# Optimization experiments

Hardware: AMD Instinct MI355X
Metric: run time of the kernel (lower is better)

The kernel has to match this reference:

```python
import jax, jax.numpy as jnp
import numpy as np

GRID_DIMS = (64, 64, 64)
GRID_LOWER = np.array([0.0, 0.0, 0.0], np.float32)
GRID_STEPS = np.array([0.015625, 0.015625, 0.015625], np.float32)
RADIUS = 0.03125
STENCIL = 2  # ceil(radius / step)


def _poly6(d2, h):
    # standard SPH poly6 smoothing kernel: 315/(64 pi h^9) (h^2 - d^2)^3, d <= h
    c = np.float32(315.0 / (64.0 * np.pi * h ** 9))
    return jnp.where(d2 <= h * h, c * (h * h - d2) ** 3, 0.0)


def particles2grid(locs, data, density):
    # locs [B,N,3], data [B,N,C], density [B,N] -> grid [B,X,Y,Z,C]
    B, N, _ = locs.shape
    C = data.shape[-1]
    X, Y, Z = GRID_DIMS
    dims = jnp.array(GRID_DIMS, jnp.int32)
    r = jnp.arange(-STENCIL, STENCIL + 1)
    offs = jnp.stack(jnp.meshgrid(r, r, r, indexing='ij'), -1).reshape(-1, 3)  # [K,3]
    base = jnp.floor((locs - GRID_LOWER) / GRID_STEPS).astype(jnp.int32)        # [B,N,3]
    cells = base[:, :, None, :] + offs                                          # [B,N,K,3]
    centers = GRID_LOWER + (cells.astype(locs.dtype) + 0.5) * GRID_STEPS
    d2 = jnp.sum((centers - locs[:, :, None, :]) ** 2, -1)                      # [B,N,K]
    w = _poly6(d2, RADIUS)
    w = jnp.where(jnp.all((cells >= 0) & (cells < dims), -1), w, 0.0)
    contrib = w[..., None] * (data / density[..., None])[:, :, None, :]         # [B,N,K,C]
    cells = jnp.clip(cells, 0, dims - 1)
    flat = (cells[..., 0] * Y + cells[..., 1]) * Z + cells[..., 2]              # [B,N,K]

    def splat(f, c):
        return jnp.zeros((X * Y * Z, C), data.dtype).at[f.reshape(-1)].add(c.reshape(-1, C))

    return jax.vmap(splat)(flat, contrib).reshape(B, X, Y, Z, C)


def grid2particles(grid, locs):
    # trilinear interpolation of grid [B,X,Y,Z,C] at particle locations [B,N,3]
    B, X, Y, Z, C = grid.shape
    dims = jnp.array([X, Y, Z], jnp.int32)
    pos = (locs - GRID_LOWER) / GRID_STEPS - 0.5                                # cell-center coords
    i0 = jnp.floor(pos).astype(jnp.int32)
    frac = pos - i0.astype(locs.dtype)
    gflat = grid.reshape(B, X * Y * Z, C)
    gather = jax.vmap(lambda g, f: g[f])                                        # [B,N] -> [B,N,C]
    out = jnp.zeros((B, locs.shape[1], C), grid.dtype)
    for dx in (0, 1):
        for dy in (0, 1):
            for dz in (0, 1):
                off = jnp.array([dx, dy, dz], jnp.int32)
                idx = i0 + off
                wd = jnp.where(off == 1, frac, 1.0 - frac)                      # [B,N,3]
                w = wd[..., 0] * wd[..., 1] * wd[..., 2]
                w = jnp.where(jnp.all((idx >= 0) & (idx < dims), -1), w, 0.0)
                idx = jnp.clip(idx, 0, dims - 1)
                flat = (idx[..., 0] * Y + idx[..., 1]) * Z + idx[..., 2]
                out = out + w[..., None] * gather(gflat, flat)
    return out


def conv3d(x, w, b):
    y = jax.lax.conv_general_dilated(x, w, (1, 1, 1), 'SAME',
                                     dimension_numbers=('NCDHW', 'OIDHW', 'NCDHW'))
    return y + b[None, :, None, None, None]


def prelu(x, a):
    return jnp.where(x >= 0, x, a * x)


def setup_inputs() -> dict:
    key = jax.random.key(0)
    ks = jax.random.split(key, 8)
    B, N = 2, 32768
    Cin, K, Cout = 4, 32, 4
    s = lambda fan: np.float32(1.0 / np.sqrt(fan * 27))
    return {
        'locs': jax.random.uniform(ks[0], (B, N, 3), jnp.float32),
        'data': jax.random.normal(ks[1], (B, N, Cin), jnp.float32),
        'density': jax.random.uniform(ks[2], (B, N), jnp.float32, 0.5, 1.5),
        'W0': jax.random.normal(ks[3], (K, Cin, 3, 3, 3), jnp.float32) * s(Cin),
        'b0': jnp.zeros((K,), jnp.float32),
        'W1': jax.random.normal(ks[4], (K, K, 3, 3, 3), jnp.float32) * s(K),
        'b1': jnp.zeros((K,), jnp.float32),
        'W2': jax.random.normal(ks[5], (K, K, 3, 3, 3), jnp.float32) * s(K),
        'b2': jnp.zeros((K,), jnp.float32),
        'W3': jax.random.normal(ks[6], (Cout, K, 3, 3, 3), jnp.float32) * s(K),
        'b3': jnp.zeros((Cout,), jnp.float32),
        'a0': jnp.full((1,), 0.25, jnp.float32),
        'a1': jnp.full((1,), 0.25, jnp.float32),
        'a2': jnp.full((1,), 0.25, jnp.float32),
    }


def reference(locs, data, density, W0, b0, W1, b1, W2, b2, W3, b3, a0, a1, a2):
    grid = particles2grid(locs, data, density)            # [B,X,Y,Z,Cin]
    g = jnp.transpose(grid, (0, 4, 1, 2, 3))              # NCDHW
    g = prelu(conv3d(g, W0, b0), a0)
    g = prelu(conv3d(g, W1, b1), a1)
    g = prelu(conv3d(g, W2, b2), a2)
    g = conv3d(g, W3, b3)
    g = jnp.transpose(g, (0, 2, 3, 4, 1))                 # [B,X,Y,Z,Cout]
    return grid2particles(g, locs)                        # [B,N,Cout]
```

## Files before the change

kernel.cpp:

```cpp
#include <hip/hip_runtime.h>

#define BATCH 2
#define NPART 32768
#define GD 64
#define NVOX (BATCH * GD * GD * GD)

typedef unsigned short ushortT;
typedef __attribute__((ext_vector_type(8))) short short8;
typedef __attribute__((ext_vector_type(16))) float float16;

__device__ __forceinline__ float poly6_c() {
    const double H9 = 1.0 / 35184372088832.0;
    return (float)(315.0 / (64.0 * 3.14159265358979323846 * H9));
}

__device__ __forceinline__ ushortT bf16_rne(float f) {
    unsigned int u = __float_as_uint(f);
    u = (u + 0x7fffu + ((u >> 16) & 1u)) >> 16;
    return (ushortT)u;
}

__device__ __forceinline__ int imax(int a, int b) { return a > b ? a : b; }
__device__ __forceinline__ int imin(int a, int b) { return a < b ? a : b; }

__device__ __forceinline__ void load_lds16(const void* g, void* l) {
    __builtin_amdgcn_global_load_lds(
        (const __attribute__((address_space(1))) void*)g,
        (__attribute__((address_space(3))) void*)l, 16, 0, 0);
}

__device__ __forceinline__ int perm_ktL(int slot) {
    int g = slot / 6, r = slot - g * 6;
    int dy = r >> 1, p = r & 1;
    int dx = g / 3, dz = g - dx * 3;
    return (dx * 9 + dy * 3 + dz) * 2 + p;
}

__global__ __launch_bounds__(256) void prep_kernel(
    int* __restrict__ zp,
    const float* __restrict__ W0, const float* __restrict__ W1,
    const float* __restrict__ W2, const float* __restrict__ W3,
    short* __restrict__ Bp) {
    int bid = blockIdx.x, tid = threadIdx.x;
    if (bid < 513) {
        int t = bid * 256 + tid;
        if (t < 131088) zp[t] = 0;
        return;
    }
    int t = (bid - 513) * 256 + tid;
    if (t >= 176 * 512) return;
    int kt = t >> 9;
    const float* W; int O, I, CINP, ktL;
    if (kt < 14)       { W = W0; O = 32; I = 4;  CINP = 8;  ktL = kt; }
    else if (kt < 68)  { W = W1; O = 32; I = 32; CINP = 32; ktL = perm_ktL(kt - 14); }
    else if (kt < 122) { W = W2; O = 32; I = 32; CINP = 32; ktL = perm_ktL(kt - 68); }
    else               { W = W3; O = 4;  I = 32; CINP = 32; ktL = perm_ktL(kt - 122); }
    int l = (t >> 3) & 63, j = t & 7;
    int n = l & 31, q = l >> 5;
    int k = ktL * 16 + 8 * q + j;
    int tap = k / CINP;
    int ic  = k - tap * CINP;
    float v = 0.f;
    if (tap < 27 && ic < I && n < O) v = W[(n * I + ic) * 27 + tap];
    Bp[t] = (short)bf16_rne(v);
}

__global__ __launch_bounds__(256) void bin_count_kernel(
    const float* __restrict__ locs, int* __restrict__ counts) {
    int t = blockIdx.x * blockDim.x + threadIdx.x;
    if (t >= BATCH * NPART) return;
    int b = t >> 15;
    int bx = ((int)floorf(locs[t * 3 + 0] * 64.0f)) >> 1;
    int by = ((int)floorf(locs[t * 3 + 1] * 64.0f)) >> 1;
    int bz = ((int)floorf(locs[t * 3 + 2] * 64.0f)) >> 1;
    atomicAdd(&counts[b * 32768 + ((bx * 32) + by) * 32 + bz], 1);
}

__global__ __launch_bounds__(256) void scanA_kernel(
    const int* __restrict__ counts, int* __restrict__ offsets,
    int* __restrict__ blockSum) {
    __shared__ int sh[256];
    int tid = threadIdx.x, g = blockIdx.x;
    int v = counts[g * 256 + tid];
    sh[tid] = v;
    __syncthreads();
    for (int off = 1; off < 256; off <<= 1) {
        int u = (tid >= off) ? sh[tid - off] : 0;
        __syncthreads();
        sh[tid] += u;
        __syncthreads();
    }
    offsets[g * 256 + tid] = sh[tid] - v;
    if (tid == 255) blockSum[g] = sh[255];
}

__global__ __launch_bounds__(256) void scanB_kernel(
    int* __restrict__ offsets, const int* __restrict__ blockSum) {
    __shared__ int sh[256];
    int tid = threadIdx.x, g = blockIdx.x;
    sh[tid] = (tid < g) ? blockSum[tid] : 0;
    __syncthreads();
    for (int off = 128; off > 0; off >>= 1) {
        if (tid < off) sh[tid] += sh[tid + off];
        __syncthreads();
    }
    offsets[g * 256 + tid] += sh[0];
    if (g == 255 && tid == 255) offsets[65536] = BATCH * NPART;
}

__global__ __launch_bounds__(256) void bin_scatter_kernel(
    const float* __restrict__ locs, const float* __restrict__ data,
    const float* __restrict__ density, const int* __restrict__ offsets,
    int* __restrict__ cursor, float* __restrict__ payload) {
    int t = blockIdx.x * blockDim.x + threadIdx.x;
    if (t >= BATCH * NPART) return;
    int b = t >> 15;
    float px = locs[t * 3 + 0];
    float py = locs[t * 3 + 1];
    float pz = locs[t * 3 + 2];
    int bx = ((int)floorf(px * 64.0f)) >> 1;
    int by = ((int)floorf(py * 64.0f)) >> 1;
    int bz = ((int)floorf(pz * 64.0f)) >> 1;
    int bb = b * 32768 + ((bx * 32) + by) * 32 + bz;
    int slot = atomicAdd(&cursor[bb], 1);
    int idx = offsets[bb] + slot;
    float inv_d = 1.0f / density[t];
    float4 p0 = {px, py, pz, data[t * 4 + 0] * inv_d};
    float4 p1 = {data[t * 4 + 1] * inv_d, data[t * 4 + 2] * inv_d,
                 data[t * 4 + 3] * inv_d, 0.f};
    *(float4*)(payload + idx * 8)     = p0;
    *(float4*)(payload + idx * 8 + 4) = p1;
}

__global__ __launch_bounds__(256) void splat_gather_kernel(
    const float* __restrict__ payload, const int* __restrict__ offsets,
    ushortT* __restrict__ g8) {
    __shared__ float plist[256 * 8];
    __shared__ int segS[36];
    __shared__ int segP[37];
    __shared__ int shTot[1];

    int wg = blockIdx.x;
    int sb = wg & 511, b = wg >> 9;
    int X0 = (sb >> 6) * 8, Y0 = ((sb >> 3) & 7) * 8, Z0 = (sb & 7) * 8;
    int tid = threadIdx.x;

    int bxlo = imax(0, (X0 - 2) >> 1), bxhi = imin(31, (X0 + 9) >> 1);
    int bylo = imax(0, (Y0 - 2) >> 1), byhi = imin(31, (Y0 + 9) >> 1);
    int bzlo = imax(0, (Z0 - 2) >> 1), bzhi = imin(31, (Z0 + 9) >> 1);
    int ny = byhi - bylo + 1;
    int ns = (bxhi - bxlo + 1) * ny;
    if (tid < ns) {
        int bx = bxlo + tid / ny, by = bylo + tid % ny;
        int row = b * 32768 + (bx * 32 + by) * 32;
        int s = offsets[row + bzlo];
        int e = offsets[row + bzhi + 1];
        segS[tid] = s;
        segP[tid] = e - s;
    }
    __syncthreads();
    if (tid == 0) {
        int p = 0;
        for (int k = 0; k < ns; ++k) { int len = segP[k]; segP[k] = p; p += len; }
        segP[ns] = p;
        shTot[0] = p;
    }
    __syncthreads();

    const float step = 0.015625f;
    const float h2 = 0.03125f * 0.03125f;
    const float cc = poly6_c();
    int total = shTot[0];

    int l = tid & 63, w = tid >> 6;
    int cx = X0 + 4 * (w >> 1) + (l >> 4);
    int cy = Y0 + 4 * (w & 1) + ((l >> 2) & 3);
    int cz0 = Z0 + (l & 3);
    float xc  = ((float)cx  + 0.5f) * step;
    float yc  = ((float)cy  + 0.5f) * step;
    float zc0 = ((float)cz0 + 0.5f) * step;
    float zc1 = zc0 + 4.0f * step;

    float a00 = 0.f, a01 = 0.f, a02 = 0.f, a03 = 0.f;
    float a10 = 0.f, a11 = 0.f, a12 = 0.f, a13 = 0.f;

    int nchunks = (total + 255) >> 8;
    for (int ch = 0; ch < nchunks; ++ch) {
        __syncthreads();
        int jj = (ch << 8) + tid;
        if (jj < total) {
            int k = 0;
            while (jj >= segP[k + 1]) ++k;
            int idx = segS[k] + (jj - segP[k]);
            *(float4*)(plist + tid * 8)     = *(const float4*)(payload + idx * 8);
            *(float4*)(plist + tid * 8 + 4) = *(const float4*)(payload + idx * 8 + 4);
        }
        __syncthreads();
        int cnt = imin(256, total - (ch << 8));
        for (int p = 0; p < cnt; ++p) {
            float4 pa = *(const float4*)(plist + p * 8);
            float dx = pa.x - xc, dy = pa.y - yc;
            float dxy2 = fmaf(dy, dy, dx * dx);
            if (!__any(dxy2 <= h2)) continue;
            float4 pv = *(const float4*)(plist + p * 8 + 4);
            float dz0 = pa.z - zc0;
            float d20 = fmaf(dz0, dz0, dxy2);
            float u0 = fmaxf(h2 - d20, 0.f);
            float w0 = (cc * u0) * (u0 * u0);
            a00 = fmaf(w0, pa.w, a00);
            a01 = fmaf(w0, pv.x, a01);
            a02 = fmaf(w0, pv.y, a02);
            a03 = fmaf(w0, pv.z, a03);
            float dz1 = pa.z - zc1;
            float d21 = fmaf(dz1, dz1, dxy2);
            float u1 = fmaxf(h2 - d21, 0.f);
            float w1 = (cc * u1) * (u1 * u1);
            a10 = fmaf(w1, pa.w, a10);
            a11 = fmaf(w1, pv.x, a11);
            a12 = fmaf(w1, pv.y, a12);
            a13 = fmaf(w1, pv.z, a13);
        }
    }

    size_t cellBase = (size_t)(((b * 64 + cx) * 64 + cy) * 64);
    short8 o;
    o[0] = (short)bf16_rne(a00); o[1] = (short)bf16_rne(a01);
    o[2] = (short)bf16_rne(a02); o[3] = (short)bf16_rne(a03);
    o[4] = 0; o[5] = 0; o[6] = 0; o[7] = 0;
    *(short8*)(g8 + (cellBase + cz0) * 8) = o;
    o[0] = (short)bf16_rne(a10); o[1] = (short)bf16_rne(a11);
    o[2] = (short)bf16_rne(a12); o[3] = (short)bf16_rne(a13);
    *(short8*)(g8 + (cellBase + cz0 + 4) * 8) = o;
}

template <int ICG, int KT, bool FINAL>
__global__ __launch_bounds__(256, (ICG == 1) ? 3 : 2) void mfma_conv_kernel(
    const ushortT* __restrict__ in, const short* __restrict__ Bpack,
    const float* __restrict__ bias, const float* __restrict__ alpha,
    const float* __restrict__ zguard, void* __restrict__ outv) {
    constexpr int CIN = ICG * 8;
    constexpr int NCH = 36 * ICG * 34;
    __shared__ short lds[NCH * 8];
    int wg = ((blockIdx.x & 7) << 7) | (blockIdx.x >> 3);
    int zh = wg & 1, yq = (wg >> 1) & 15, xp = (wg >> 5) & 15, b = wg >> 9;
    int X0 = xp * 4, Y0 = yq * 4, Z0 = zh * 32;
    int tid = threadIdx.x;

    const ushortT* inb = in + (size_t)b * (64 * 64 * 64 * CIN);
#pragma unroll
    for (int it = 0; it < (NCH + 255) / 256; ++it) {
        int ccid = it * 256 + tid;
        if (ccid < NCH) {
            int col = ccid / (ICG * 34);
            int rem = ccid - col * (ICG * 34);
            int icg = rem / 34;
            int zi  = rem - icg * 34;
            int gx = X0 + col / 6 - 1;
            int gy = Y0 + col % 6 - 1;
            int gz = Z0 + zi - 1;
            const void* src = (const void*)zguard;
            if ((unsigned)gx < 64u && (unsigned)gy < 64u && (unsigned)gz < 64u)
                src = (const void*)(inb + ((size_t)(((gx * 64) + gy) * 64 + gz)) * CIN + icg * 8);
            load_lds16(src, (void*)(lds + ccid * 8));
        }
    }
    __syncthreads();

    int l = tid & 63, w = tid >> 6;
    int n = l & 31, q = l >> 5;

    float bval = FINAL ? (n < 4 ? bias[n] : 0.f) : bias[n];
    float16 acc0, acc1, acc2, acc3;
#pragma unroll
    for (int r = 0; r < 16; ++r) {
        acc0[r] = bval; acc1[r] = bval; acc2[r] = bval; acc3[r] = bval;
    }

    const short* bp = Bpack + (size_t)l * 8;
    int laneZ = (l & 31) * 8;

    short8 bf[4];
#pragma unroll
    for (int i = 0; i < 4; ++i) bf[i] = *(const short8*)(bp + i * 512);

    if constexpr (ICG == 1) {
#pragma unroll
        for (int kt = 0; kt < KT; ++kt) {
            short8 bcur = bf[kt & 3];
            if (kt + 4 < KT) bf[kt & 3] = *(const short8*)(bp + (kt + 4) * 512);
            int tap0 = kt * 2, tap1 = kt * 2 + 1;
            if (tap1 > 26) tap1 = 26;
            int dx0 = tap0 / 9, r0 = tap0 - dx0 * 9, dy0 = r0 / 3, dz0 = r0 - dy0 * 3;
            int dx1 = tap1 / 9, r1 = tap1 - dx1 * 9, dy1 = r1 / 3, dz1 = r1 - dy1 * 3;
#define AOFS1(c) (q ? ((((w + dx1) * 6 + ((c) + dy1)) * 34 + dz1) * 8) \
                    : ((((w + dx0) * 6 + ((c) + dy0)) * 34 + dz0) * 8))
            short8 a0 = *(const short8*)(lds + AOFS1(0) + laneZ);
            short8 a1 = *(const short8*)(lds + AOFS1(1) + laneZ);
            short8 a2 = *(const short8*)(lds + AOFS1(2) + laneZ);
            short8 a3 = *(const short8*)(lds + AOFS1(3) + laneZ);
#undef AOFS1
            __builtin_amdgcn_s_setprio(1);
            acc0 = __builtin_amdgcn_mfma_f32_32x32x16_bf16(a0, bcur, acc0, 0, 0, 0);
            acc1 = __builtin_amdgcn_mfma_f32_32x32x16_bf16(a1, bcur, acc1, 0, 0, 0);
            acc2 = __builtin_amdgcn_mfma_f32_32x32x16_bf16(a2, bcur, acc2, 0, 0, 0);
            acc3 = __builtin_amdgcn_mfma_f32_32x32x16_bf16(a3, bcur, acc3, 0, 0, 0);
            __builtin_amdgcn_s_setprio(0);
        }
    } else {
#pragma unroll
        for (int g = 0; g < 9; ++g) {
            int dx = g / 3, dz = g - dx * 3;
            short8 fr[6][2];
#pragma unroll
            for (int col = 0; col < 6; ++col) {
#pragma unroll
                for (int p = 0; p < 2; ++p) {
                    int icg = p * 2 + q;
                    int ofs = ((((w + dx) * 6 + col) * ICG + icg) * 34 + dz) * 8;
                    fr[col][p] = *(const short8*)(lds + ofs + laneZ);
                }
            }
#pragma unroll
            for (int dy = 0; dy < 3; ++dy) {
#pragma unroll
                for (int p = 0; p < 2; ++p) {
                    int kt = g * 6 + dy * 2 + p;
                    short8 bcur = bf[kt & 3];
                    if (kt + 4 < KT) bf[kt & 3] = *(const short8*)(bp + (kt + 4) * 512);
                    __builtin_amdgcn_s_setprio(1);
                    acc0 = __builtin_amdgcn_mfma_f32_32x32x16_bf16(fr[0 + dy][p], bcur, acc0, 0, 0, 0);
                    acc1 = __builtin_amdgcn_mfma_f32_32x32x16_bf16(fr[1 + dy][p], bcur, acc1, 0, 0, 0);
                    acc2 = __builtin_amdgcn_mfma_f32_32x32x16_bf16(fr[2 + dy][p], bcur, acc2, 0, 0, 0);
                    acc3 = __builtin_amdgcn_mfma_f32_32x32x16_bf16(fr[3 + dy][p], bcur, acc3, 0, 0, 0);
                    __builtin_amdgcn_s_setprio(0);
                }
            }
        }
    }

    size_t base0 = (size_t)(((b * 64 + X0 + w) * 64 + Y0) * 64) + Z0;
    if (FINAL) {
        float* out = (float*)outv;
        if (n < 4) {
#pragma unroll
            for (int r = 0; r < 16; ++r) {
                int z = (r & 3) + 8 * (r >> 2) + 4 * q;
                out[(base0 + z) * 4 + n]        = acc0[r];
                out[(base0 + 64 + z) * 4 + n]   = acc1[r];
                out[(base0 + 128 + z) * 4 + n]  = acc2[r];
                out[(base0 + 192 + z) * 4 + n]  = acc3[r];
            }
        }
    } else {
        float a = alpha[0];
        ushortT* out = (ushortT*)outv;
#pragma unroll
        for (int r = 0; r < 16; ++r) {
            int z = (r & 3) + 8 * (r >> 2) + 4 * q;
            float v0 = acc0[r]; v0 = v0 >= 0.f ? v0 : a * v0;
            out[(base0 + z) * 32 + n] = bf16_rne(v0);
            float v1 = acc1[r]; v1 = v1 >= 0.f ? v1 : a * v1;
            out[(base0 + 64 + z) * 32 + n] = bf16_rne(v1);
            float v2 = acc2[r]; v2 = v2 >= 0.f ? v2 : a * v2;
            out[(base0 + 128 + z) * 32 + n] = bf16_rne(v2);
            float v3 = acc3[r]; v3 = v3 >= 0.f ? v3 : a * v3;
            out[(base0 + 192 + z) * 32 + n] = bf16_rne(v3);
        }
    }
}

__global__ __launch_bounds__(256) void gather_kernel(
    const float* __restrict__ grid, const float* __restrict__ locs,
    float* __restrict__ out) {
    int t = blockIdx.x * blockDim.x + threadIdx.x;
    if (t >= BATCH * NPART) return;
    int b = t >> 15;

    float px = locs[t * 3 + 0] * 64.0f - 0.5f;
    float py = locs[t * 3 + 1] * 64.0f - 0.5f;
    float pz = locs[t * 3 + 2] * 64.0f - 0.5f;
    int ix = (int)floorf(px);
    int iy = (int)floorf(py);
    int iz = (int)floorf(pz);
    float fx = px - (float)ix;
    float fy = py - (float)iy;
    float fz = pz - (float)iz;

    const float* gb = grid + (size_t)b * GD * GD * GD * 4;
    float o0 = 0.f, o1 = 0.f, o2 = 0.f, o3 = 0.f;

#pragma unroll
    for (int dx = 0; dx < 2; ++dx) {
        int x = ix + dx;
        if ((unsigned)x > 63u) continue;
        float wx = dx ? fx : 1.0f - fx;
#pragma unroll
        for (int dy = 0; dy < 2; ++dy) {
            int y = iy + dy;
            if ((unsigned)y > 63u) continue;
            float wy = dy ? fy : 1.0f - fy;
#pragma unroll
            for (int dz = 0; dz < 2; ++dz) {
                int z = iz + dz;
                if ((unsigned)z > 63u) continue;
                float wz = dz ? fz : 1.0f - fz;
                float w = wx * wy * wz;
                const float4 g = *(const float4*)(gb + (size_t)(((x * GD) + y) * GD + z) * 4);
                o0 += w * g.x; o1 += w * g.y; o2 += w * g.z; o3 += w * g.w;
            }
        }
    }
    out[t * 4 + 0] = o0;
    out[t * 4 + 1] = o1;
    out[t * 4 + 2] = o2;
    out[t * 4 + 3] = o3;
}

extern "C" void kernel_launch(void* const* d_in, const int* in_sizes, int n_in,
                              void* d_out, int out_size, void* d_ws, size_t ws_size,
                              hipStream_t stream) {
    const float* locs    = (const float*)d_in[0];
    const float* data    = (const float*)d_in[1];
    const float* density = (const float*)d_in[2];
    const float* W0 = (const float*)d_in[3];
    const float* b0 = (const float*)d_in[4];
    const float* W1 = (const float*)d_in[5];
    const float* b1 = (const float*)d_in[6];
    const float* W2 = (const float*)d_in[7];
    const float* b2 = (const float*)d_in[8];
    const float* W3 = (const float*)d_in[9];
    const float* b3 = (const float*)d_in[10];
    const float* a0 = (const float*)d_in[11];
    const float* a1 = (const float*)d_in[12];
    const float* a2 = (const float*)d_in[13];
    float* out = (float*)d_out;

    char* ws = (char*)d_ws;
    ushortT* g8  = (ushortT*)(ws);
    ushortT* gA  = (ushortT*)(ws + 8388608);
    ushortT* gB  = (ushortT*)(ws + 41943040);
    float*  gF   = (float*)(ws + 75497472);
    short*  Bp   = (short*)(ws + 83886080);
    short*  Bp0  = Bp;
    short*  Bp1  = Bp + 14 * 512;
    short*  Bp2  = Bp + 68 * 512;
    short*  Bp3  = Bp + 122 * 512;
    float* zguard   = (float*)(ws + 84066240);
    int*   counts   = (int*)(ws + 84066304);
    int*   cursor   = (int*)(ws + 84328448);
    int*   offsets  = (int*)(ws + 84590592);
    int*   blockSum = (int*)(ws + 84852752);
    float* payload  = (float*)(ws + 84853888);

    prep_kernel<<<513 + 352, 256, 0, stream>>>((int*)zguard, W0, W1, W2, W3, Bp);

    bin_count_kernel<<<(BATCH * NPART) / 256, 256, 0, stream>>>(locs, counts);
    scanA_kernel<<<256, 256, 0, stream>>>(counts, offsets, blockSum);
    scanB_kernel<<<256, 256, 0, stream>>>(offsets, blockSum);
    bin_scatter_kernel<<<(BATCH * NPART) / 256, 256, 0, stream>>>(
        locs, data, density, offsets, cursor, payload);

    splat_gather_kernel<<<BATCH * 512, 256, 0, stream>>>(payload, offsets, g8);

    const int CGRID = 1024;
    mfma_conv_kernel< 1, 14, false><<<CGRID, 256, 0, stream>>>(g8, Bp0, b0, a0, zguard, gA);
    mfma_conv_kernel< 4, 54, false><<<CGRID, 256, 0, stream>>>(gA, Bp1, b1, a1, zguard, gB);
    mfma_conv_kernel< 4, 54, false><<<CGRID, 256, 0, stream>>>(gB, Bp2, b2, a2, zguard, gA);
    mfma_conv_kernel< 4, 54, true ><<<CGRID, 256, 0, stream>>>(gA, Bp3, b3, b3, zguard, gF);

    gather_kernel<<<(BATCH * NPART) / 256, 256, 0, stream>>>(gF, locs, out);
}
```

Before: 246.6 us.

## Split 32-channel conv input staging into two LDS halves to raise occupancy

For the 32-channel conv layers, the input tile is now staged into LDS in two 16-channel halves, with a barrier between them, instead of loading all channels at once. This halves the LDS footprint and cuts the live fragment registers. Launch bounds are raised to four waves-per-EU for every variant. The weight packing in the prep kernel is reordered to match the new half-major K order. The costs are a serialized reload-and-sync phase between the halves, less latency hiding inside a block, and possible register spills under the tighter launch bound.

```diff
diff --git a/kernel.cpp b/kernel.cpp
--- a/kernel.cpp
+++ b/kernel.cpp
@@ -27,13 +27,6 @@
     __builtin_amdgcn_global_load_lds(
         (const __attribute__((address_space(1))) void*)g,
         (__attribute__((address_space(3))) void*)l, 16, 0, 0);
-}
-
-__device__ __forceinline__ int perm_ktL(int slot) {
-    int g = slot / 6, r = slot - g * 6;
-    int dy = r >> 1, p = r & 1;
-    int dx = g / 3, dz = g - dx * 3;
-    return (dx * 9 + dy * 3 + dz) * 2 + p;
 }
 
 __global__ __launch_bounds__(256) void prep_kernel(
@@ -50,18 +43,25 @@
     int t = (bid - 513) * 256 + tid;
     if (t >= 176 * 512) return;
     int kt = t >> 9;
-    const float* W; int O, I, CINP, ktL;
-    if (kt < 14)       { W = W0; O = 32; I = 4;  CINP = 8;  ktL = kt; }
-    else if (kt < 68)  { W = W1; O = 32; I = 32; CINP = 32; ktL = perm_ktL(kt - 14); }
-    else if (kt < 122) { W = W2; O = 32; I = 32; CINP = 32; ktL = perm_ktL(kt - 68); }
-    else               { W = W3; O = 4;  I = 32; CINP = 32; ktL = perm_ktL(kt - 122); }
     int l = (t >> 3) & 63, j = t & 7;
     int n = l & 31, q = l >> 5;
-    int k = ktL * 16 + 8 * q + j;
-    int tap = k / CINP;
-    int ic  = k - tap * CINP;
     float v = 0.f;
-    if (tap < 27 && ic < I && n < O) v = W[(n * I + ic) * 27 + tap];
+    if (kt < 14) {
+        int k = kt * 16 + 8 * q + j;
+        int tap = k >> 3, ic = k & 7;
+        if (tap < 27 && ic < 4) v = W0[(n * 4 + ic) * 27 + tap];
+    } else {
+        const float* W; int O, s;
+        if (kt < 68)       { W = W1; O = 32; s = kt - 14; }
+        else if (kt < 122) { W = W2; O = 32; s = kt - 68; }
+        else               { W = W3; O = 4;  s = kt - 122; }
+        int h = s / 27, ss = s - h * 27;
+        int gI = ss / 3, dy = ss - gI * 3;
+        int dx = gI / 3, dz = gI - dx * 3;
+        int tap = dx * 9 + dy * 3 + dz;
+        int ic = h * 16 + q * 8 + j;
+        if (n < O) v = W[(n * 32 + ic) * 27 + tap];
+    }
     Bp[t] = (short)bf16_rne(v);
 }
 
@@ -234,12 +234,12 @@
 }
 
 template <int ICG, int KT, bool FINAL>
-__global__ __launch_bounds__(256, (ICG == 1) ? 3 : 2) void mfma_conv_kernel(
+__global__ __launch_bounds__(256, 4) void mfma_conv_kernel(
     const ushortT* __restrict__ in, const short* __restrict__ Bpack,
     const float* __restrict__ bias, const float* __restrict__ alpha,
     const float* __restrict__ zguard, void* __restrict__ outv) {
     constexpr int CIN = ICG * 8;
-    constexpr int NCH = 36 * ICG * 34;
+    constexpr int NCH = (ICG == 1) ? (36 * 34) : (36 * 2 * 34);
     __shared__ short lds[NCH * 8];
     int wg = ((blockIdx.x & 7) << 7) | (blockIdx.x >> 3);
     int zh = wg & 1, yq = (wg >> 1) & 15, xp = (wg >> 5) & 15, b = wg >> 9;
@@ -247,24 +247,6 @@
     int tid = threadIdx.x;
 
     const ushortT* inb = in + (size_t)b * (64 * 64 * 64 * CIN);
-#pragma unroll
-    for (int it = 0; it < (NCH + 255) / 256; ++it) {
-        int ccid = it * 256 + tid;
-        if (ccid < NCH) {
-            int col = ccid / (ICG * 34);
-            int rem = ccid - col * (ICG * 34);
-            int icg = rem / 34;
-            int zi  = rem - icg * 34;
-            int gx = X0 + col / 6 - 1;
-            int gy = Y0 + col % 6 - 1;
-            int gz = Z0 + zi - 1;
-            const void* src = (const void*)zguard;
-            if ((unsigned)gx < 64u && (unsigned)gy < 64u && (unsigned)gz < 64u)
-                src = (const void*)(inb + ((size_t)(((gx * 64) + gy) * 64 + gz)) * CIN + icg * 8);
-            load_lds16(src, (void*)(lds + ccid * 8));
-        }
-    }
-    __syncthreads();
 
     int l = tid & 63, w = tid >> 6;
     int n = l & 31, q = l >> 5;
@@ -284,6 +266,22 @@
     for (int i = 0; i < 4; ++i) bf[i] = *(const short8*)(bp + i * 512);
 
     if constexpr (ICG == 1) {
+#pragma unroll
+        for (int it = 0; it < (NCH + 255) / 256; ++it) {
+            int ccid = it * 256 + tid;
+            if (ccid < NCH) {
+                int col = ccid / 34;
+                int zi  = ccid - col * 34;
+                int gx = X0 + col / 6 - 1;
+                int gy = Y0 + col % 6 - 1;
+                int gz = Z0 + zi - 1;
+                const void* src = (const void*)zguard;
+                if ((unsigned)gx < 64u && (unsigned)gy < 64u && (unsigned)gz < 64u)
+                    src = (const void*)(inb + ((size_t)(((gx * 64) + gy) * 64 + gz)) * CIN);
+                load_lds16(src, (void*)(lds + ccid * 8));
+            }
+        }
+        __syncthreads();
 #pragma unroll
         for (int kt = 0; kt < KT; ++kt) {
             short8 bcur = bf[kt & 3];
@@ -308,30 +306,46 @@
         }
     } else {
 #pragma unroll
-        for (int g = 0; g < 9; ++g) {
-            int dx = g / 3, dz = g - dx * 3;
-            short8 fr[6][2];
-#pragma unroll
-            for (int col = 0; col < 6; ++col) {
-#pragma unroll
-                for (int p = 0; p < 2; ++p) {
-                    int icg = p * 2 + q;
-                    int ofs = ((((w + dx) * 6 + col) * ICG + icg) * 34 + dz) * 8;
-                    fr[col][p] = *(const short8*)(lds + ofs + laneZ);
+        for (int h = 0; h < 2; ++h) {
+            if (h) __syncthreads();
+#pragma unroll
+            for (int it = 0; it < (NCH + 255) / 256; ++it) {
+                int ccid = it * 256 + tid;
+                if (ccid < NCH) {
+                    int col = ccid / 68;
+                    int rem = ccid - col * 68;
+                    int icg2 = rem / 34;
+                    int zi   = rem - icg2 * 34;
+                    int gx = X0 + col / 6 - 1;
+                    int gy = Y0 + col % 6 - 1;
+                    int gz = Z0 + zi - 1;
+                    const void* src = (const void*)zguard;
+                    if ((unsigned)gx < 64u && (unsigned)gy < 64u && (unsigned)gz < 64u)
+                        src = (const void*)(inb +
+                            ((size_t)(((gx * 64) + gy) * 64 + gz)) * CIN + (h * 2 + icg2) * 8);
+                    load_lds16(src, (void*)(lds + ccid * 8));
                 }
             }
-#pragma unroll
-            for (int dy = 0; dy < 3; ++dy) {
-#pragma unroll
-                for (int p = 0; p < 2; ++p) {
-                    int kt = g * 6 + dy * 2 + p;
+            __syncthreads();
+#pragma unroll
+            for (int g = 0; g < 9; ++g) {
+                int dx = g / 3, dz = g - dx * 3;
+                short8 fr[6];
+#pragma unroll
+                for (int col = 0; col < 6; ++col) {
+                    int ofs = ((((w + dx) * 6 + col) * 2 + q) * 34 + dz) * 8;
+                    fr[col] = *(const short8*)(lds + ofs + laneZ);
+                }
+#pragma unroll
+                for (int dy = 0; dy < 3; ++dy) {
+                    int kt = h * 27 + g * 3 + dy;
                     short8 bcur = bf[kt & 3];
                     if (kt + 4 < KT) bf[kt & 3] = *(const short8*)(bp + (kt + 4) * 512);
                     __builtin_amdgcn_s_setprio(1);
-                    acc0 = __builtin_amdgcn_mfma_f32_32x32x16_bf16(fr[0 + dy][p], bcur, acc0, 0, 0, 0);
-                    acc1 = __builtin_amdgcn_mfma_f32_32x32x16_bf16(fr[1 + dy][p], bcur, acc1, 0, 0, 0);
-                    acc2 = __builtin_amdgcn_mfma_f32_32x32x16_bf16(fr[2 + dy][p], bcur, acc2, 0, 0, 0);
-                    acc3 = __builtin_amdgcn_mfma_f32_32x32x16_bf16(fr[3 + dy][p], bcur, acc3, 0, 0, 0);
+                    acc0 = __builtin_amdgcn_mfma_f32_32x32x16_bf16(fr[0 + dy], bcur, acc0, 0, 0, 0);
+                    acc1 = __builtin_amdgcn_mfma_f32_32x32x16_bf16(fr[1 + dy], bcur, acc1, 0, 0, 0);
+                    acc2 = __builtin_amdgcn_mfma_f32_32x32x16_bf16(fr[2 + dy], bcur, acc2, 0, 0, 0);
+                    acc3 = __builtin_amdgcn_mfma_f32_32x32x16_bf16(fr[3 + dy], bcur, acc3, 0, 0, 0);
                     __builtin_amdgcn_s_setprio(0);
                 }
             }
```

Result: slower. 269.2 us (+9.2%).
